# Optimization experiments

Hardware: AMD Instinct MI355X
Metric: run time of the kernel (lower is better)

Reference implementation:

```python
import jax, jax.numpy as jnp
import numpy as np

D = 1024   # dims
H = 16     # heads
HD = D // H  # head_dim = 64
F = HD // 2  # rotary frequency count


def _layernorm(x, g, b, eps=1e-5):
    m = x.mean(-1, keepdims=True)
    v = jnp.mean((x - m) ** 2, axis=-1, keepdims=True)
    return (x - m) * jax.lax.rsqrt(v + eps) * g + b


def _freq_base():
    # mask=None branch of rotary._compute_freqs: mel-style frequencies
    mel_max = 2595.0 * np.log10(1.0 + 4000.0 / 200.0)
    scale = 10.0 ** (np.linspace(0.0, mel_max, F) / 2595.0) - 1.0
    return jnp.asarray(200.0 * scale / 1000.0, dtype=jnp.float32)  # [F]


def _rope_polar(xh, radius, theta):
    # xh: [b,h,c,hd]; radius: [b,c] (learned per-token magnitude); theta: [c,F]
    # complex multiply of interleaved pairs by r*exp(i*theta)
    b_, h_, c_, hd_ = xh.shape
    xp = xh.reshape(b_, h_, c_, F, 2)
    xr, xi = xp[..., 0], xp[..., 1]
    cos = jnp.cos(theta)[None, None]  # [1,1,c,F]
    sin = jnp.sin(theta)[None, None]
    r = radius[:, None, :, None]      # [b,1,c,1]
    out_r = r * (xr * cos - xi * sin)
    out_i = r * (xr * sin + xi * cos)
    return jnp.stack([out_r, out_i], axis=-1).reshape(b_, h_, c_, hd_)


def setup_inputs() -> dict:
    key = jax.random.key(0)
    ks = jax.random.split(key, 6)
    B, C = 2, 2048
    s = 0.02
    return {
        "x": jax.random.normal(ks[0], (B, C, D), jnp.float32),
        "ln_q_g": jnp.ones((D,), jnp.float32),
        "ln_q_b": jnp.zeros((D,), jnp.float32),
        "Wq": jax.random.normal(ks[1], (D, D), jnp.float32) * s,
        "bq": jnp.zeros((D,), jnp.float32),
        "ln_kv_g": jnp.ones((D,), jnp.float32),
        "ln_kv_b": jnp.zeros((D,), jnp.float32),
        "Wkv": jax.random.normal(ks[2], (D, 2 * D), jnp.float32) * s,
        "bkv": jnp.zeros((2 * D,), jnp.float32),
        "Wout": jax.random.normal(ks[3], (D, D), jnp.float32) * s,
        "bout": jnp.zeros((D,), jnp.float32),
        "lnh_g": jnp.ones((HD,), jnp.float32),
        "lnh_b": jnp.zeros((HD,), jnp.float32),
        "Wr": jax.random.normal(ks[4], (D, 1), jnp.float32) * s,
        "br": jnp.zeros((1,), jnp.float32),
    }


def reference(x, ln_q_g, ln_q_b, Wq, bq, ln_kv_g, ln_kv_b, Wkv, bkv,
              Wout, bout, lnh_g, lnh_b, Wr, br):
    B, C, _ = x.shape
    # q path: norm -> linear -> [b,h,c,d]
    q = (_layernorm(x, ln_q_g, ln_q_b) @ Wq + bq).reshape(B, C, H, HD).transpose(0, 2, 1, 3)
    # kv path: norm -> linear -> [2,b,h,c,d]
    kv = (_layernorm(x, ln_kv_g, ln_kv_b) @ Wkv + bkv).reshape(B, C, 2, H, HD).transpose(2, 0, 3, 1, 4)
    k, v = kv[0], kv[1]
    # polar RoPE with learned per-token radius (xa = x for both q and k)
    t = jnp.arange(C, dtype=jnp.float32)
    theta = t[:, None] * _freq_base()[None, :]               # [C,F]
    per_step = (x @ Wr + br)[..., 0]                         # [B,C]
    radius = jnp.clip(per_step / 100.0, 0.5, 2.0)
    q = _rope_polar(q, radius, theta)
    k = _rope_polar(k, radius, theta)
    # per-head LayerNorm fused into SDPA inputs
    qn = _layernorm(q, lnh_g, lnh_b)
    kn = _layernorm(k, lnh_g, lnh_b)
    # non-causal SDPA (torch default scale = 1/sqrt(head_dim))
    logits = jnp.einsum('bhqd,bhkd->bhqk', qn, kn) / jnp.sqrt(jnp.float32(HD))
    attn = jax.nn.softmax(logits, axis=-1)
    o = jnp.einsum('bhqk,bhkd->bhqd', attn, v)
    o = o.transpose(0, 2, 1, 3).reshape(B, C, D)
    return o @ Wout + bout
```

## Files before the change

### kernel.cpp

```cpp
#include <hip/hip_runtime.h>
#include <math.h>

#define D_MODEL 1024
#define NHEADS  16
#define HEADD   64
#define NFREQ   32
#define BATCH   2
#define CSEQ    2048
#define NROWS   (BATCH*CSEQ)
#define NQKV    (3*D_MODEL)

typedef _Float16 half8  __attribute__((ext_vector_type(8)));
typedef _Float16 half4v __attribute__((ext_vector_type(4)));
typedef float    f32x4  __attribute__((ext_vector_type(4)));

__device__ __forceinline__ void async16(void* lds, const void* g)
{
    __builtin_amdgcn_global_load_lds((const __attribute__((address_space(1))) unsigned int*)g,
                                     (__attribute__((address_space(3))) unsigned int*)lds,
                                     16, 0, 0);
}

__global__ __launch_bounds__(256) void prep_misc_kernel(
    float2* __restrict__ cs,
    const float* __restrict__ bq, const float* __restrict__ bkv, float* __restrict__ be)
{
    int bid = blockIdx.x;
    int tid = threadIdx.x;
    if (bid < 256) {
        int i = bid * 256 + tid;
        int c = i >> 5, f = i & (NFREQ - 1);
        double mel_max = 2595.0 * log10(21.0);
        double step    = mel_max / (double)(NFREQ - 1);
        double freq    = 200.0 * (pow(10.0, step * (double)f / 2595.0) - 1.0) / 1000.0;
        float fr = (float)freq;
        float th = (float)c * fr;
        float s, co;
        sincosf(th, &s, &co);
        cs[i] = make_float2(co, s);
    } else {
        int i = (bid - 256) * 256 + tid;
        if (i < D_MODEL) be[i] = bq[i];
        else if (i < NQKV) be[i] = bkv[i - D_MODEL];
    }
}

__global__ void transpose_all_kernel(
    const float* __restrict__ Wq,  const float* __restrict__ Wkv,
    const float* __restrict__ Wout,
    const float* __restrict__ gq,  const float* __restrict__ bqf,
    const float* __restrict__ gkv, const float* __restrict__ bkvf,
    _Float16* __restrict__ WqkvT, _Float16* __restrict__ WoutT,
    float* __restrict__ bias_acc)
{
    const float* in; _Float16* out; int R, C, rowoff;
    const float* scale; const float* bfold;
    int id = blockIdx.x, bx, by;
    if (id < 1024) {
        in = Wq; out = WqkvT; R = D_MODEL; C = D_MODEL; rowoff = 0;
        scale = gq; bfold = bqf;
        bx = (id & 31) * 32; by = (id >> 5) * 32;
    } else if (id < 3072) {
        int t = id - 1024;
        in = Wkv; out = WqkvT; R = D_MODEL; C = 2 * D_MODEL; rowoff = D_MODEL;
        scale = gkv; bfold = bkvf;
        bx = (t & 63) * 32; by = (t >> 6) * 32;
    } else {
        int t = id - 3072;
        in = Wout; out = WoutT; R = D_MODEL; C = D_MODEL; rowoff = 0;
        scale = nullptr; bfold = nullptr;
        bx = (t & 31) * 32; by = (t >> 5) * 32;
    }

    __shared__ float tb[32][33];
    __shared__ float part[4][32];
    int tx = threadIdx.x, ty = threadIdx.y;
    #pragma unroll
    for (int i = ty; i < 32; i += 8)
        tb[i][tx] = in[(size_t)(by + i) * C + bx + tx];
    __syncthreads();
    float sc = scale ? scale[by + tx] : 1.f;
    #pragma unroll
    for (int i = ty; i < 32; i += 8)
        out[(size_t)(rowoff + bx + i) * R + by + tx] = (_Float16)(tb[tx][i] * sc);
    if (bfold) {
        float p = 0.f;
        #pragma unroll
        for (int i = ty; i < 32; i += 8)
            p += bfold[by + i] * tb[i][tx];
        p += __shfl_xor(p, 32);
        if ((ty & 1) == 0) part[ty >> 1][tx] = p;
        __syncthreads();
        if (ty == 0)
            atomicAdd(&bias_acc[rowoff + bx + tx],
                      part[0][tx] + part[1][tx] + part[2][tx] + part[3][tx]);
    }
}

__global__ __launch_bounds__(256) void ln_radius_kernel(
    const float* __restrict__ x,
    const float* __restrict__ Wr,  const float* __restrict__ br,
    _Float16* __restrict__ xn, float* __restrict__ radius)
{
    int row = blockIdx.x;
    int tid = threadIdx.x;
    float4 xv = ((const float4*)(x + (size_t)row * D_MODEL))[tid];
    float4 wv = ((const float4*)Wr)[tid];
    float s  = xv.x + xv.y + xv.z + xv.w;
    float ss = xv.x*xv.x + xv.y*xv.y + xv.z*xv.z + xv.w*xv.w;
    float dr = xv.x*wv.x + xv.y*wv.y + xv.z*wv.z + xv.w*wv.w;
    #pragma unroll
    for (int off = 1; off < 64; off <<= 1) {
        s  += __shfl_xor(s, off);
        ss += __shfl_xor(ss, off);
        dr += __shfl_xor(dr, off);
    }
    __shared__ float red[3][4];
    int w = tid >> 6, lane = tid & 63;
    if (lane == 0) { red[0][w] = s; red[1][w] = ss; red[2][w] = dr; }
    __syncthreads();
    s  = red[0][0] + red[0][1] + red[0][2] + red[0][3];
    ss = red[1][0] + red[1][1] + red[1][2] + red[1][3];
    float mean = s * (1.f / D_MODEL);
    float var  = ss * (1.f / D_MODEL) - mean * mean;
    float rinv = rsqrtf(var + 1e-5f);
    half4v o4 = { (_Float16)((xv.x - mean) * rinv), (_Float16)((xv.y - mean) * rinv),
                  (_Float16)((xv.z - mean) * rinv), (_Float16)((xv.w - mean) * rinv) };
    *(half4v*)&xn[(size_t)row * D_MODEL + tid * 4] = o4;
    if (tid == 0) {
        float drt = red[2][0] + red[2][1] + red[2][2] + red[2][3];
        float p = (drt + br[0]) * 0.01f;
        radius[row] = fminf(fmaxf(p, 0.5f), 2.0f);
    }
}

__device__ __forceinline__ void gemm_core32p(
    const _Float16* __restrict__ A, const _Float16* __restrict__ B,
    int bm, int bn, int K, _Float16* As, _Float16* Bs, f32x4 (*acc)[4])
{
    int tid = threadIdx.x, lane = tid & 63, w = tid >> 6;
    int wm = w >> 1, wn = w & 1;
    int l15 = lane & 15, lg = lane >> 4;
    int sr  = lane >> 2;
    int sch = lane & 3;

    auto stage = [&](int buf, int k0) {
        #pragma unroll
        for (int i = 0; i < 2; ++i) {
            int seg = w * 2 + i;
            int row = seg * 16 + sr;
            async16(&As[buf * 4096 + seg * 512], &A[(size_t)(bm + row) * K + k0 + sch * 8]);
            async16(&Bs[buf * 4096 + seg * 512], &B[(size_t)(bn + row) * K + k0 + sch * 8]);
        }
    };

    int nt = K >> 5;
    stage(0, 0);
    stage(1, 32);

    for (int t = 0; t < nt; ++t) {
        if (t + 1 < nt) asm volatile("s_waitcnt vmcnt(4)" ::: "memory");
        else            asm volatile("s_waitcnt vmcnt(0)" ::: "memory");
        __builtin_amdgcn_sched_barrier(0);
        __builtin_amdgcn_s_barrier();
        __builtin_amdgcn_sched_barrier(0);
        if (t + 2 < nt) stage((t + 2) % 3, (t + 2) << 5);

        const _Float16* Ab = &As[(t % 3) * 4096];
        const _Float16* Bb = &Bs[(t % 3) * 4096];
        half8 af[4], bf[4];
        #pragma unroll
        for (int m = 0; m < 4; ++m)
            af[m] = *(const half8*)&Ab[(wm * 64 + m * 16 + l15) * 32 + lg * 8];
        #pragma unroll
        for (int n = 0; n < 4; ++n)
            bf[n] = *(const half8*)&Bb[(wn * 64 + n * 16 + l15) * 32 + lg * 8];
        #pragma unroll
        for (int m = 0; m < 4; ++m)
            #pragma unroll
            for (int n = 0; n < 4; ++n)
                acc[m][n] = __builtin_amdgcn_mfma_f32_16x16x32_f16(af[m], bf[n], acc[m][n], 0, 0, 0);
    }
}

__global__ __launch_bounds__(256, 3) void gemm_qkv_kernel(
    const _Float16* __restrict__ xn,  const _Float16* __restrict__ WT,
    const float* __restrict__ bias_eff,
    const float* __restrict__ radius, const float2* __restrict__ cs_tab,
    const float* __restrict__ lnh_g,  const float* __restrict__ lnh_b,
    _Float16* __restrict__ qn, _Float16* __restrict__ kn, _Float16* __restrict__ vT)
{
    __shared__ _Float16 As[3 * 4096];
    __shared__ _Float16 Bs[3 * 4096];
    int orig = blockIdx.x;
    int wg = (orig & 7) * 96 + (orig >> 3);
    int bm = (wg / 24) * 128;
    int bn = (wg % 24) * 128;

    f32x4 acc[4][4];
    f32x4 z = {0.f, 0.f, 0.f, 0.f};
    #pragma unroll
    for (int m = 0; m < 4; ++m)
        #pragma unroll
        for (int n = 0; n < 4; ++n) acc[m][n] = z;

    gemm_core32p(xn, WT, bm, bn, D_MODEL, As, Bs, acc);

    int tid = threadIdx.x, lane = tid & 63, w = tid >> 6;
    int wm = w >> 1, wn = w & 1;
    int l15 = lane & 15, lg = lane >> 4;
    int colbase = bn + wn * 64;

    float bb4[4];
    #pragma unroll
    for (int n = 0; n < 4; ++n) bb4[n] = bias_eff[colbase + n * 16 + l15];

    if (colbase >= 2 * D_MODEL) {
        int vcolb = colbase - 2 * D_MODEL;
        int h = vcolb >> 6;
        #pragma unroll
        for (int m = 0; m < 4; ++m) {
            int row0 = bm + wm * 64 + m * 16 + lg * 4;
            int b = row0 >> 11, c = row0 & (CSEQ - 1);
            #pragma unroll
            for (int n = 0; n < 4; ++n) {
                int d = n * 16 + l15;
                half4v v4 = { (_Float16)(acc[m][n][0] + bb4[n]),
                              (_Float16)(acc[m][n][1] + bb4[n]),
                              (_Float16)(acc[m][n][2] + bb4[n]),
                              (_Float16)(acc[m][n][3] + bb4[n]) };
                *(half4v*)&vT[((size_t)(b * NHEADS + h) * HEADD + d) * CSEQ + c] = v4;
            }
        }
        return;
    }

    bool isq = colbase < D_MODEL;
    int h = (colbase & (D_MODEL - 1)) >> 6;
    _Float16* dst = isq ? qn : kn;
    float qs = isq ? 0.125f : 1.f;
    bool im = (l15 & 1) != 0;

    float g4[4], bh4[4];
    #pragma unroll
    for (int n = 0; n < 4; ++n) {
        g4[n]  = lnh_g[n * 16 + l15];
        bh4[n] = lnh_b[n * 16 + l15];
    }

    #pragma unroll
    for (int m = 0; m < 4; ++m)
        #pragma unroll
        for (int r = 0; r < 4; ++r) {
            int row = bm + wm * 64 + m * 16 + lg * 4 + r;
            int b = row >> 11, c = row & (CSEQ - 1);
            float rr = radius[row];
            float vals[4];
            float s = 0.f, ss = 0.f;
            #pragma unroll
            for (int n = 0; n < 4; ++n) {
                float v0 = acc[m][n][r] + bb4[n];
                float pr = __shfl_xor(v0, 1);
                float2 cs = cs_tab[c * NFREQ + ((n * 16 + l15) >> 1)];
                float xr_ = im ? pr : v0;
                float xi_ = im ? v0 : pr;
                float rot = im ? rr * (xr_ * cs.y + xi_ * cs.x)
                               : rr * (xr_ * cs.x - xi_ * cs.y);
                vals[n] = rot;
                s += rot; ss += rot * rot;
            }
            #pragma unroll
            for (int off = 1; off < 16; off <<= 1) {
                s  += __shfl_xor(s, off);
                ss += __shfl_xor(ss, off);
            }
            float mean = s * (1.f / 64.f);
            float var  = ss * (1.f / 64.f) - mean * mean;
            float ri   = rsqrtf(var + 1e-5f);
            size_t base = ((size_t)(b * NHEADS + h) * CSEQ + c) * HEADD;
            #pragma unroll
            for (int n = 0; n < 4; ++n) {
                float o = ((vals[n] - mean) * ri * g4[n] + bh4[n]) * qs;
                dst[base + n * 16 + l15] = (_Float16)o;
            }
        }
}

__global__ __launch_bounds__(256, 3) void gemm_out_kernel(
    const _Float16* __restrict__ A, const _Float16* __restrict__ BT,
    const float* __restrict__ bias, float* __restrict__ C)
{
    __shared__ _Float16 As[3 * 4096];
    __shared__ _Float16 Bs[3 * 4096];
    int orig = blockIdx.x;
    int wg = (orig & 7) * 32 + (orig >> 3);
    int bm = (wg >> 3) * 128;
    int bn = (wg & 7) * 128;

    f32x4 acc[4][4];
    f32x4 z = {0.f, 0.f, 0.f, 0.f};
    #pragma unroll
    for (int m = 0; m < 4; ++m)
        #pragma unroll
        for (int n = 0; n < 4; ++n) acc[m][n] = z;

    gemm_core32p(A, BT, bm, bn, D_MODEL, As, Bs, acc);

    int tid = threadIdx.x, lane = tid & 63, w = tid >> 6;
    int wm = w >> 1, wn = w & 1;
    int l15 = lane & 15, lg = lane >> 4;
    #pragma unroll
    for (int m = 0; m < 4; ++m) {
        int row = bm + wm * 64 + m * 16 + lg * 4;
        #pragma unroll
        for (int n = 0; n < 4; ++n) {
            int col = bn + wn * 64 + n * 16 + l15;
            float bb = bias[col];
            #pragma unroll
            for (int r = 0; r < 4; ++r)
                C[(size_t)(row + r) * D_MODEL + col] = acc[m][n][r] + bb;
        }
    }
}

#define KVB 64
#define NT  (CSEQ / KVB)

__global__ __launch_bounds__(256, 4) void attn_kernel(
    const _Float16* __restrict__ qn, const _Float16* __restrict__ kn,
    const _Float16* __restrict__ vT, _Float16* __restrict__ o)
{
    __shared__ _Float16 KsB[2][KVB * 64];
    __shared__ _Float16 VsB[2][KVB * 64];
    __shared__ _Float16 P[4][16 * 64];
    int tid = threadIdx.x, lane = tid & 63, w = tid >> 6;
    int l15 = lane & 15, lg = lane >> 4;

    int orig = blockIdx.x;
    int wg   = (orig & 7) * 128 + (orig >> 3);
    int bh   = wg >> 5;
    int qc   = wg & 31;
    int q0   = qc * 64 + w * 16;

    const _Float16* qh = qn + (size_t)bh * CSEQ * HEADD;
    const _Float16* kh = kn + (size_t)bh * CSEQ * HEADD;
    const _Float16* vh = vT + (size_t)bh * HEADD * CSEQ;

    half8 aq[2];
    #pragma unroll
    for (int ks = 0; ks < 2; ++ks)
        aq[ks] = *(const half8*)&qh[(size_t)(q0 + l15) * HEADD + ks * 32 + lg * 8];

    f32x4 z = {0.f, 0.f, 0.f, 0.f};
    f32x4 oacc[4];
    #pragma unroll
    for (int d4 = 0; d4 < 4; ++d4) oacc[d4] = z;
    float mrun = -1e30f, lrun = 0.f;

    int srow_in = lane >> 3;
    int csrc    = (lane & 7) ^ srow_in;
    int lsw     = l15 & 7;

    auto stage = [&](int buf, int kt) {
        int k0 = kt * KVB;
        #pragma unroll
        for (int i = 0; i < 2; ++i) {
            int seg = w * 2 + i;
            int r = seg * 8 + srow_in;
            async16(&KsB[buf][seg * 512], &kh[(size_t)(k0 + r) * HEADD + csrc * 8]);
            async16(&VsB[buf][seg * 512], &vh[(size_t)r * CSEQ + k0 + csrc * 8]);
        }
    };

    stage(0, 0);
    __syncthreads();
    int cur = 0;

    for (int kt = 0; kt < NT; ++kt) {
        if (kt + 1 < NT) stage(cur ^ 1, kt + 1);

        f32x4 st[4];
        #pragma unroll
        for (int n = 0; n < 4; ++n) st[n] = z;
        #pragma unroll
        for (int ks = 0; ks < 2; ++ks) {
            half8 ak[4];
            #pragma unroll
            for (int n = 0; n < 4; ++n) {
                int row = n * 16 + l15;
                int ch = (ks * 4 + lg) ^ (row & 7);
                ak[n] = *(const half8*)&KsB[cur][row * 64 + ch * 8];
            }
            #pragma unroll
            for (int n = 0; n < 4; ++n)
                st[n] = __builtin_amdgcn_mfma_f32_16x16x32_f16(ak[n], aq[ks], st[n], 0, 0, 0);
        }

        float mx0 = fmaxf(fmaxf(st[0][0], st[0][1]), fmaxf(st[0][2], st[0][3]));
        float mx1 = fmaxf(fmaxf(st[1][0], st[1][1]), fmaxf(st[1][2], st[1][3]));
        float mx2 = fmaxf(fmaxf(st[2][0], st[2][1]), fmaxf(st[2][2], st[2][3]));
        float mx3 = fmaxf(fmaxf(st[3][0], st[3][1]), fmaxf(st[3][2], st[3][3]));
        float tmax = fmaxf(fmaxf(mx0, mx1), fmaxf(mx2, mx3));
        tmax = fmaxf(tmax, __shfl_xor(tmax, 16));
        tmax = fmaxf(tmax, __shfl_xor(tmax, 32));

        if (!__all(tmax <= mrun + 8.f)) {
            float nm = fmaxf(mrun, tmax);
            float sc = __expf(mrun - nm);
            mrun = nm;
            lrun *= sc;
            float scO[4];
            #pragma unroll
            for (int r = 0; r < 4; ++r) scO[r] = __shfl(sc, lg * 4 + r);
            #pragma unroll
            for (int d4 = 0; d4 < 4; ++d4)
                #pragma unroll
                for (int r = 0; r < 4; ++r) oacc[d4][r] *= scO[r];
        }

        float ps = 0.f;
        #pragma unroll
        for (int n = 0; n < 4; ++n)
            #pragma unroll
            for (int r = 0; r < 4; ++r) {
                float e = __expf(st[n][r] - mrun);
                st[n][r] = e;
                ps += e;
            }
        ps += __shfl_xor(ps, 16);
        ps += __shfl_xor(ps, 32);
        lrun += ps;

        #pragma unroll
        for (int n = 0; n < 4; ++n) {
            half4v pk;
            #pragma unroll
            for (int r = 0; r < 4; ++r) pk[r] = (_Float16)st[n][r];
            int t  = n * 2 + (lg >> 1);
            int tp = t ^ lsw;
            *(half4v*)&P[w][l15 * 64 + tp * 8 + (lg & 1) * 4] = pk;
        }

        #pragma unroll
        for (int ks = 0; ks < 2; ++ks) {
            int tp2 = (ks * 4 + lg) ^ lsw;
            half8 ap = *(const half8*)&P[w][l15 * 64 + tp2 * 8];
            half8 bv[4];
            #pragma unroll
            for (int d4 = 0; d4 < 4; ++d4) {
                int row = d4 * 16 + l15;
                int ch = (ks * 4 + lg) ^ (row & 7);
                bv[d4] = *(const half8*)&VsB[cur][row * 64 + ch * 8];
            }
            #pragma unroll
            for (int d4 = 0; d4 < 4; ++d4)
                oacc[d4] = __builtin_amdgcn_mfma_f32_16x16x32_f16(ap, bv[d4], oacc[d4], 0, 0, 0);
        }

        __syncthreads();
        cur ^= 1;
    }

    int b = bh >> 4, h = bh & 15;
    #pragma unroll
    for (int r = 0; r < 4; ++r) {
        float lr = __shfl(lrun, lg * 4 + r);
        float inv = 1.f / lr;
        int c = q0 + lg * 4 + r;
        size_t base = ((size_t)b * CSEQ + c) * D_MODEL + h * HEADD;
        #pragma unroll
        for (int d4 = 0; d4 < 4; ++d4)
            o[base + d4 * 16 + l15] = (_Float16)(oacc[d4][r] * inv);
    }
}

extern "C" void kernel_launch(void* const* d_in, const int* in_sizes, int n_in,
                              void* d_out, int out_size, void* d_ws, size_t ws_size,
                              hipStream_t stream)
{
    (void)in_sizes; (void)n_in; (void)out_size; (void)ws_size;
    const float* x      = (const float*)d_in[0];
    const float* ln_q_g = (const float*)d_in[1];
    const float* ln_q_b = (const float*)d_in[2];
    const float* Wq     = (const float*)d_in[3];
    const float* bq     = (const float*)d_in[4];
    const float* ln_kv_g= (const float*)d_in[5];
    const float* ln_kv_b= (const float*)d_in[6];
    const float* Wkv    = (const float*)d_in[7];
    const float* bkv    = (const float*)d_in[8];
    const float* Wout   = (const float*)d_in[9];
    const float* bout   = (const float*)d_in[10];
    const float* lnh_g  = (const float*)d_in[11];
    const float* lnh_b  = (const float*)d_in[12];
    const float* Wr     = (const float*)d_in[13];
    const float* br     = (const float*)d_in[14];
    float* out = (float*)d_out;

    char* ws = (char*)d_ws;
    size_t off = 0;
    auto alloc = [&](size_t bytes) -> void* {
        void* p = ws + off;
        off += (bytes + 255) & ~(size_t)255;
        return p;
    };
    _Float16* WqkvT  = (_Float16*)alloc((size_t)NQKV * D_MODEL * 2);
    _Float16* WoutT  = (_Float16*)alloc((size_t)D_MODEL * D_MODEL * 2);
    float*    bias_e = (float*)   alloc((size_t)NQKV * 4);
    float*    radius = (float*)   alloc((size_t)NROWS * 4);
    float2*   cs_tab = (float2*)  alloc((size_t)CSEQ * NFREQ * 8);
    _Float16* vT     = (_Float16*)alloc((size_t)BATCH * NHEADS * HEADD * CSEQ * 2);
    _Float16* xn     = (_Float16*)alloc((size_t)NROWS * D_MODEL * 2);
    _Float16* qn     = (_Float16*)alloc((size_t)NROWS * D_MODEL * 2);
    _Float16* kn     = (_Float16*)alloc((size_t)NROWS * D_MODEL * 2);
    _Float16* o_h    = (_Float16*)alloc((size_t)NROWS * D_MODEL * 2);

    hipLaunchKernelGGL(prep_misc_kernel, dim3(268), dim3(256), 0, stream,
                       cs_tab, bq, bkv, bias_e);
    hipLaunchKernelGGL(transpose_all_kernel, dim3(4096), dim3(32, 8), 0, stream,
                       Wq, Wkv, Wout, ln_q_g, ln_q_b, ln_kv_g, ln_kv_b,
                       WqkvT, WoutT, bias_e);
    hipLaunchKernelGGL(ln_radius_kernel, dim3(NROWS), dim3(256), 0, stream,
                       x, Wr, br, xn, radius);
    hipLaunchKernelGGL(gemm_qkv_kernel, dim3(768), dim3(256), 0, stream,
                       xn, WqkvT, bias_e, radius, cs_tab, lnh_g, lnh_b, qn, kn, vT);
    hipLaunchKernelGGL(attn_kernel, dim3(BATCH*NHEADS*CSEQ/64), dim3(256), 0, stream,
                       qn, kn, vT, o_h);
    hipLaunchKernelGGL(gemm_out_kernel, dim3(256), dim3(256), 0, stream,
                       o_h, WoutT, bout, out);
}
```

Baseline: 150.0 us.

## Keep attention probabilities in registers and retile output GEMM to 128x64

The attention kernel no longer writes P to LDS. It computes O^T with 16x16x16 MFMAs, so the exp'd scores in the accumulator layout feed straight in as the B operand. This removes the LDS round-trip and per-row shuffles, and the store becomes vectorized half4 writes, at the cost of twice as many smaller MFMAs. Separately, the output GEMM switches to 128x64 tiles with an inline triple-buffered async pipeline and 512 blocks, which should improve occupancy and CU coverage.

```diff
diff --git a/kernel.cpp b/kernel.cpp
--- a/kernel.cpp
+++ b/kernel.cpp
@@ -286,35 +286,73 @@
         }
 }
 
-__global__ __launch_bounds__(256, 3) void gemm_out_kernel(
+__global__ __launch_bounds__(256, 4) void gemm_out_kernel(
     const _Float16* __restrict__ A, const _Float16* __restrict__ BT,
     const float* __restrict__ bias, float* __restrict__ C)
 {
     __shared__ _Float16 As[3 * 4096];
-    __shared__ _Float16 Bs[3 * 4096];
+    __shared__ _Float16 Bs[3 * 2048];
     int orig = blockIdx.x;
-    int wg = (orig & 7) * 32 + (orig >> 3);
-    int bm = (wg >> 3) * 128;
-    int bn = (wg & 7) * 128;
-
-    f32x4 acc[4][4];
-    f32x4 z = {0.f, 0.f, 0.f, 0.f};
-    #pragma unroll
-    for (int m = 0; m < 4; ++m)
-        #pragma unroll
-        for (int n = 0; n < 4; ++n) acc[m][n] = z;
-
-    gemm_core32p(A, BT, bm, bn, D_MODEL, As, Bs, acc);
+    int wg = (orig & 7) * 64 + (orig >> 3);
+    int bm = (wg >> 4) * 128;
+    int bn = (wg & 15) * 64;
 
     int tid = threadIdx.x, lane = tid & 63, w = tid >> 6;
     int wm = w >> 1, wn = w & 1;
     int l15 = lane & 15, lg = lane >> 4;
+    int sr  = lane >> 2;
+    int sch = lane & 3;
+
+    f32x4 acc[4][2];
+    f32x4 z = {0.f, 0.f, 0.f, 0.f};
+    #pragma unroll
+    for (int m = 0; m < 4; ++m)
+        #pragma unroll
+        for (int n = 0; n < 2; ++n) acc[m][n] = z;
+
+    auto stage = [&](int buf, int k0) {
+        #pragma unroll
+        for (int i = 0; i < 2; ++i) {
+            int seg = w * 2 + i;
+            int row = seg * 16 + sr;
+            async16(&As[buf * 4096 + seg * 512], &A[(size_t)(bm + row) * D_MODEL + k0 + sch * 8]);
+        }
+        int brow = w * 16 + sr;
+        async16(&Bs[buf * 2048 + w * 512], &BT[(size_t)(bn + brow) * D_MODEL + k0 + sch * 8]);
+    };
+
+    stage(0, 0);
+    stage(1, 32);
+    for (int t = 0; t < 32; ++t) {
+        if (t + 1 < 32) asm volatile("s_waitcnt vmcnt(3)" ::: "memory");
+        else            asm volatile("s_waitcnt vmcnt(0)" ::: "memory");
+        __builtin_amdgcn_sched_barrier(0);
+        __builtin_amdgcn_s_barrier();
+        __builtin_amdgcn_sched_barrier(0);
+        if (t + 2 < 32) stage((t + 2) % 3, (t + 2) << 5);
+
+        const _Float16* Ab = &As[(t % 3) * 4096];
+        const _Float16* Bb = &Bs[(t % 3) * 2048];
+        half8 af[4], bf[2];
+        #pragma unroll
+        for (int m = 0; m < 4; ++m)
+            af[m] = *(const half8*)&Ab[(wm * 64 + m * 16 + l15) * 32 + lg * 8];
+        #pragma unroll
+        for (int n = 0; n < 2; ++n)
+            bf[n] = *(const half8*)&Bb[(wn * 32 + n * 16 + l15) * 32 + lg * 8];
+        #pragma unroll
+        for (int m = 0; m < 4; ++m)
+            #pragma unroll
+            for (int n = 0; n < 2; ++n)
+                acc[m][n] = __builtin_amdgcn_mfma_f32_16x16x32_f16(af[m], bf[n], acc[m][n], 0, 0, 0);
+    }
+
     #pragma unroll
     for (int m = 0; m < 4; ++m) {
         int row = bm + wm * 64 + m * 16 + lg * 4;
         #pragma unroll
-        for (int n = 0; n < 4; ++n) {
-            int col = bn + wn * 64 + n * 16 + l15;
+        for (int n = 0; n < 2; ++n) {
+            int col = bn + wn * 32 + n * 16 + l15;
             float bb = bias[col];
             #pragma unroll
             for (int r = 0; r < 4; ++r)
@@ -332,7 +370,6 @@
 {
     __shared__ _Float16 KsB[2][KVB * 64];
     __shared__ _Float16 VsB[2][KVB * 64];
-    __shared__ _Float16 P[4][16 * 64];
     int tid = threadIdx.x, lane = tid & 63, w = tid >> 6;
     int l15 = lane & 15, lg = lane >> 4;
 
@@ -354,12 +391,12 @@
     f32x4 z = {0.f, 0.f, 0.f, 0.f};
     f32x4 oacc[4];
     #pragma unroll
-    for (int d4 = 0; d4 < 4; ++d4) oacc[d4] = z;
+    for (int db = 0; db < 4; ++db) oacc[db] = z;
     float mrun = -1e30f, lrun = 0.f;
 
     int srow_in = lane >> 3;
     int csrc    = (lane & 7) ^ srow_in;
-    int lsw     = l15 & 7;
+    int l7      = l15 & 7;
 
     auto stage = [&](int buf, int kt) {
         int k0 = kt * KVB;
@@ -409,68 +446,50 @@
             float sc = __expf(mrun - nm);
             mrun = nm;
             lrun *= sc;
-            float scO[4];
-            #pragma unroll
-            for (int r = 0; r < 4; ++r) scO[r] = __shfl(sc, lg * 4 + r);
-            #pragma unroll
-            for (int d4 = 0; d4 < 4; ++d4)
-                #pragma unroll
-                for (int r = 0; r < 4; ++r) oacc[d4][r] *= scO[r];
-        }
-
+            #pragma unroll
+            for (int db = 0; db < 4; ++db) oacc[db] *= sc;
+        }
+
+        half4v bp[4];
         float ps = 0.f;
         #pragma unroll
-        for (int n = 0; n < 4; ++n)
-            #pragma unroll
-            for (int r = 0; r < 4; ++r) {
-                float e = __expf(st[n][r] - mrun);
-                st[n][r] = e;
-                ps += e;
+        for (int n = 0; n < 4; ++n) {
+            float e0 = __expf(st[n][0] - mrun);
+            float e1 = __expf(st[n][1] - mrun);
+            float e2 = __expf(st[n][2] - mrun);
+            float e3 = __expf(st[n][3] - mrun);
+            ps += (e0 + e1) + (e2 + e3);
+            half4v pk = { (_Float16)e0, (_Float16)e1, (_Float16)e2, (_Float16)e3 };
+            bp[n] = pk;
+        }
+        lrun += ps;
+
+        #pragma unroll
+        for (int n = 0; n < 4; ++n) {
+            #pragma unroll
+            for (int db = 0; db < 4; ++db) {
+                int row = db * 16 + l15;
+                int ch = (n * 2 + (lg >> 1)) ^ (row & 7);
+                half4v av = *(const half4v*)&VsB[cur][row * 64 + ch * 8 + (lg & 1) * 4];
+                oacc[db] = __builtin_amdgcn_mfma_f32_16x16x16f16(av, bp[n], oacc[db], 0, 0, 0);
             }
-        ps += __shfl_xor(ps, 16);
-        ps += __shfl_xor(ps, 32);
-        lrun += ps;
-
-        #pragma unroll
-        for (int n = 0; n < 4; ++n) {
-            half4v pk;
-            #pragma unroll
-            for (int r = 0; r < 4; ++r) pk[r] = (_Float16)st[n][r];
-            int t  = n * 2 + (lg >> 1);
-            int tp = t ^ lsw;
-            *(half4v*)&P[w][l15 * 64 + tp * 8 + (lg & 1) * 4] = pk;
-        }
-
-        #pragma unroll
-        for (int ks = 0; ks < 2; ++ks) {
-            int tp2 = (ks * 4 + lg) ^ lsw;
-            half8 ap = *(const half8*)&P[w][l15 * 64 + tp2 * 8];
-            half8 bv[4];
-            #pragma unroll
-            for (int d4 = 0; d4 < 4; ++d4) {
-                int row = d4 * 16 + l15;
-                int ch = (ks * 4 + lg) ^ (row & 7);
-                bv[d4] = *(const half8*)&VsB[cur][row * 64 + ch * 8];
-            }
-            #pragma unroll
-            for (int d4 = 0; d4 < 4; ++d4)
-                oacc[d4] = __builtin_amdgcn_mfma_f32_16x16x32_f16(ap, bv[d4], oacc[d4], 0, 0, 0);
         }
 
         __syncthreads();
         cur ^= 1;
     }
 
+    lrun += __shfl_xor(lrun, 16);
+    lrun += __shfl_xor(lrun, 32);
+    float inv = 1.f / lrun;
     int b = bh >> 4, h = bh & 15;
-    #pragma unroll
-    for (int r = 0; r < 4; ++r) {
-        float lr = __shfl(lrun, lg * 4 + r);
-        float inv = 1.f / lr;
-        int c = q0 + lg * 4 + r;
-        size_t base = ((size_t)b * CSEQ + c) * D_MODEL + h * HEADD;
-        #pragma unroll
-        for (int d4 = 0; d4 < 4; ++d4)
-            o[base + d4 * 16 + l15] = (_Float16)(oacc[d4][r] * inv);
+    int c = q0 + l15;
+    size_t base = ((size_t)b * CSEQ + c) * D_MODEL + h * HEADD;
+    #pragma unroll
+    for (int db = 0; db < 4; ++db) {
+        half4v ov = { (_Float16)(oacc[db][0] * inv), (_Float16)(oacc[db][1] * inv),
+                      (_Float16)(oacc[db][2] * inv), (_Float16)(oacc[db][3] * inv) };
+        *(half4v*)&o[base + db * 16 + lg * 4] = ov;
     }
 }
 
@@ -525,6 +544,6 @@
                        xn, WqkvT, bias_e, radius, cs_tab, lnh_g, lnh_b, qn, kn, vT);
     hipLaunchKernelGGL(attn_kernel, dim3(BATCH*NHEADS*CSEQ/64), dim3(256), 0, stream,
                        qn, kn, vT, o_h);
-    hipLaunchKernelGGL(gemm_out_kernel, dim3(256), dim3(256), 0, stream,
+    hipLaunchKernelGGL(gemm_out_kernel, dim3(512), dim3(256), 0, stream,
                        o_h, WoutT, bout, out);
 }
```

After: 146.6 us. 2.3% less time.
